# Kernel optimization log

Measured on AMD Instinct MI355X. Metric: run time of the kernel, lower is better.

## Reference

```python
import jax, jax.numpy as jnp
import numpy as np

LN_EPS = 1e-5
ATTN_THRESH = 0.0005


def _layernorm(x, g, b):
    mu = jnp.mean(x, axis=-1, keepdims=True)
    var = jnp.mean((x - mu) ** 2, axis=-1, keepdims=True)
    return (x - mu) / jnp.sqrt(var + LN_EPS) * g + b


def setup_inputs() -> dict:
    key = jax.random.key(0)
    ks = jax.random.split(key, 10)
    B, P, X, C = 4, 1024, 8192, 1024
    return {
        "feat": jax.random.normal(ks[0], (B, P, C), dtype=jnp.float32),
        "mem_k": jax.random.normal(ks[1], (B, X, C), dtype=jnp.float32),
        "mem_v": jax.random.normal(ks[2], (B, X, C), dtype=jnp.float32),
        "mem_c": jax.random.uniform(ks[3], (B, X, 1), dtype=jnp.float32),
        "mem_attn": jnp.zeros((B, X, 1), dtype=jnp.float32),
        "g_q": jax.random.uniform(ks[4], (C,), dtype=jnp.float32, minval=0.5, maxval=1.5),
        "b_q": jax.random.normal(ks[5], (C,), dtype=jnp.float32) * 0.02,
        "g_k": jax.random.uniform(ks[6], (C,), dtype=jnp.float32, minval=0.5, maxval=1.5),
        "b_k": jax.random.normal(ks[7], (C,), dtype=jnp.float32) * 0.02,
        "g_v": jax.random.uniform(ks[8], (C,), dtype=jnp.float32, minval=0.5, maxval=1.5),
        "b_v": jax.random.normal(ks[9], (C,), dtype=jnp.float32) * 0.02,
    }


def reference(feat, mem_k, mem_v, mem_c, mem_attn, g_q, b_q, g_k, b_k, g_v, b_v):
    # SpatialMemory.memory_read with res=True
    C = feat.shape[-1]
    q = _layernorm(feat, g_q, b_q)                      # [B,P,C]
    k = _layernorm(mem_k, g_k, b_k)                     # [B,X,C]
    affinity = jnp.einsum('bpc,bxc->bpx', q, k)
    affinity = affinity / jnp.sqrt(jnp.asarray(C, jnp.float32))
    # confidence scaling: mem_c viewed as [B,1,X]
    affinity = affinity * jnp.swapaxes(mem_c, 1, 2)
    attn = jax.nn.softmax(affinity, axis=-1)            # [B,P,X]
    # threshold sparsify + renormalize
    attn = jnp.where(attn < ATTN_THRESH, jnp.zeros((), attn.dtype), attn)
    attn = attn / jnp.sum(attn, axis=-1, keepdims=True)
    v = _layernorm(mem_v, g_v, b_v)                     # [B,X,C]
    out = jnp.einsum('bpx,bxc->bpc', attn, v) + feat    # residual
    return out
```

## Files before the change

kernel.cpp:

```cpp
#include <hip/hip_runtime.h>

typedef __attribute__((ext_vector_type(8))) _Float16 half8;
typedef __attribute__((ext_vector_type(4))) _Float16 half4v;
typedef __attribute__((ext_vector_type(4))) float f32x4;
typedef __attribute__((ext_vector_type(16))) float f32x16;

__device__ __forceinline__ void gll16(const void* g, void* l) {
  __builtin_amdgcn_global_load_lds(
      (const __attribute__((address_space(1))) unsigned int*)g,
      (__attribute__((address_space(3))) unsigned int*)l, 16, 0, 0);
}

__device__ __forceinline__ float h2f(unsigned short hb) {
  _Float16 h;
  __builtin_memcpy(&h, &hb, 2);
  return (float)h;
}

__global__ __launch_bounds__(256) void ln_cast_f16(
    const float* __restrict__ x, const float* __restrict__ g,
    const float* __restrict__ b, _Float16* __restrict__ y) {
  const int C = 1024;
  size_t row = blockIdx.x;
  int t = threadIdx.x;
  const float4* xr = (const float4*)(x + row * C);
  float4 v = xr[t];
  float s = v.x + v.y + v.z + v.w;
  float s2 = v.x * v.x + v.y * v.y + v.z * v.z + v.w * v.w;
#pragma unroll
  for (int off = 1; off < 64; off <<= 1) {
    s += __shfl_xor(s, off, 64);
    s2 += __shfl_xor(s2, off, 64);
  }
  __shared__ float ps[4], ps2[4];
  int wave = t >> 6, lane = t & 63;
  if (lane == 0) { ps[wave] = s; ps2[wave] = s2; }
  __syncthreads();
  s = ps[0] + ps[1] + ps[2] + ps[3];
  s2 = ps2[0] + ps2[1] + ps2[2] + ps2[3];
  float mu = s * (1.0f / C);
  float var = s2 * (1.0f / C) - mu * mu;
  float rstd = rsqrtf(var + 1e-5f);
  float4 gv = ((const float4*)g)[t];
  float4 bv = ((const float4*)b)[t];
  half4v o;
  o.x = (_Float16)((v.x - mu) * rstd * gv.x + bv.x);
  o.y = (_Float16)((v.y - mu) * rstd * gv.y + bv.y);
  o.z = (_Float16)((v.z - mu) * rstd * gv.z + bv.z);
  o.w = (_Float16)((v.w - mu) * rstd * gv.w + bv.w);
  ((half4v*)(y + row * C))[t] = o;
}

__global__ __launch_bounds__(256) void ln_cast_i8(
    const float* __restrict__ x, const float* __restrict__ g,
    const float* __restrict__ b, char* __restrict__ y,
    float* __restrict__ yscale) {
  const int C = 1024;
  size_t row = blockIdx.x;
  int t = threadIdx.x;
  const float4* xr = (const float4*)(x + row * C);
  float4 v = xr[t];
  float s = v.x + v.y + v.z + v.w;
  float s2 = v.x * v.x + v.y * v.y + v.z * v.z + v.w * v.w;
#pragma unroll
  for (int off = 1; off < 64; off <<= 1) {
    s += __shfl_xor(s, off, 64);
    s2 += __shfl_xor(s2, off, 64);
  }
  __shared__ float ps[4], ps2[4], pm[4];
  int wave = t >> 6, lane = t & 63;
  if (lane == 0) { ps[wave] = s; ps2[wave] = s2; }
  __syncthreads();
  s = ps[0] + ps[1] + ps[2] + ps[3];
  s2 = ps2[0] + ps2[1] + ps2[2] + ps2[3];
  float mu = s * (1.0f / C);
  float var = s2 * (1.0f / C) - mu * mu;
  float rstd = rsqrtf(var + 1e-5f);
  float4 gv = ((const float4*)g)[t];
  float4 bv = ((const float4*)b)[t];
  float o0 = (v.x - mu) * rstd * gv.x + bv.x;
  float o1 = (v.y - mu) * rstd * gv.y + bv.y;
  float o2 = (v.z - mu) * rstd * gv.z + bv.z;
  float o3 = (v.w - mu) * rstd * gv.w + bv.w;
  float mx = fmaxf(fmaxf(fabsf(o0), fabsf(o1)), fmaxf(fabsf(o2), fabsf(o3)));
#pragma unroll
  for (int off = 1; off < 64; off <<= 1) mx = fmaxf(mx, __shfl_xor(mx, off, 64));
  if (lane == 0) pm[wave] = mx;
  __syncthreads();
  mx = fmaxf(fmaxf(pm[0], pm[1]), fmaxf(pm[2], pm[3]));
  mx = fmaxf(mx, 1e-20f);
  float inv = 127.0f / mx;
  int q0 = (int)rintf(o0 * inv), q1 = (int)rintf(o1 * inv);
  int q2 = (int)rintf(o2 * inv), q3 = (int)rintf(o3 * inv);
  unsigned pk = ((unsigned)(q0 & 0xff)) | ((unsigned)(q1 & 0xff) << 8) |
                ((unsigned)(q2 & 0xff) << 16) | ((unsigned)(q3 & 0xff) << 24);
  ((unsigned*)(y + row * C))[t] = pk;
  if (t == 0) yscale[row] = mx * (1.0f / 127.0f);
}

__global__ __launch_bounds__(512, 2) void gemm_qk_256(
    const _Float16* __restrict__ A,
    const _Float16* __restrict__ Bm,
    _Float16* __restrict__ Sm,
    const float* __restrict__ conf)
{
  const int N = 8192, K = 1024;
  int bz = blockIdx.z;
  const _Float16* Ab = A + (size_t)bz * 1024 * K;
  const _Float16* Bb = Bm + (size_t)bz * (size_t)N * K;
  _Float16* Sb = Sm + (size_t)bz * 1024 * N;

  __shared__ _Float16 lA[4 * 8192];
  __shared__ _Float16 lB[4 * 8192];

  int tid = threadIdx.x;
  int wave = tid >> 6, lane = tid & 63;
  int wm = wave >> 2, wn = wave & 3;
  int lr = lane & 31, lk = lane >> 5;
  int m0 = blockIdx.y * 256, n0 = blockIdx.x * 256;

  f32x16 acc[4][2];
#pragma unroll
  for (int i = 0; i < 4; ++i)
#pragma unroll
    for (int j = 0; j < 2; ++j)
#pragma unroll
      for (int e = 0; e < 16; ++e) acc[i][j][e] = 0.f;

  int r = tid & 255, c0 = tid >> 8;
  const _Float16* gA = Ab + (size_t)(m0 + r) * K + c0 * 8;
  const _Float16* gB = Bb + (size_t)(n0 + r) * K + c0 * 8;
  int dA = c0 * 2048 + r * 8;

  auto stage = [&](int t) {
    int bo = (t & 3) * 8192;
    const _Float16* ga = gA + t * 32;
    const _Float16* gb = gB + t * 32;
    gll16(ga, &lA[bo + dA]);
    gll16(ga + 16, &lA[bo + dA + 4096]);
    gll16(gb, &lB[bo + dA]);
    gll16(gb + 16, &lB[bo + dA + 4096]);
  };

  auto compute = [&](int bo) {
#pragma unroll
    for (int ks = 0; ks < 2; ++ks) {
      const _Float16* la = &lA[bo + (ks * 2 + lk) * 2048 + (wm * 128 + lr) * 8];
      const _Float16* lb = &lB[bo + (ks * 2 + lk) * 2048 + (wn * 64 + lr) * 8];
      half8 a0 = *(const half8*)(la);
      half8 a1 = *(const half8*)(la + 256);
      half8 a2 = *(const half8*)(la + 512);
      half8 a3 = *(const half8*)(la + 768);
      half8 b0 = *(const half8*)(lb);
      half8 b1 = *(const half8*)(lb + 256);
      __builtin_amdgcn_s_setprio(1);
      acc[0][0] = __builtin_amdgcn_mfma_f32_32x32x16_f16(a0, b0, acc[0][0], 0, 0, 0);
      acc[1][0] = __builtin_amdgcn_mfma_f32_32x32x16_f16(a1, b0, acc[1][0], 0, 0, 0);
      acc[2][0] = __builtin_amdgcn_mfma_f32_32x32x16_f16(a2, b0, acc[2][0], 0, 0, 0);
      acc[3][0] = __builtin_amdgcn_mfma_f32_32x32x16_f16(a3, b0, acc[3][0], 0, 0, 0);
      acc[0][1] = __builtin_amdgcn_mfma_f32_32x32x16_f16(a0, b1, acc[0][1], 0, 0, 0);
      acc[1][1] = __builtin_amdgcn_mfma_f32_32x32x16_f16(a1, b1, acc[1][1], 0, 0, 0);
      acc[2][1] = __builtin_amdgcn_mfma_f32_32x32x16_f16(a2, b1, acc[2][1], 0, 0, 0);
      acc[3][1] = __builtin_amdgcn_mfma_f32_32x32x16_f16(a3, b1, acc[3][1], 0, 0, 0);
      __builtin_amdgcn_s_setprio(0);
    }
  };

  stage(0);
  stage(1);
  stage(2);

#pragma unroll 4
  for (int kt = 0; kt < 29; ++kt) {
    stage(kt + 3);
    __builtin_amdgcn_s_waitcnt(0xF7C);
    __builtin_amdgcn_s_barrier();
    __builtin_amdgcn_sched_barrier(0);
    compute((kt & 3) * 8192);
    __builtin_amdgcn_sched_barrier(0);
    __builtin_amdgcn_s_barrier();
  }
  __builtin_amdgcn_s_waitcnt(0xF78);
  __builtin_amdgcn_s_barrier();
  __builtin_amdgcn_sched_barrier(0);
  compute(1 * 8192);
  __builtin_amdgcn_sched_barrier(0);
  __builtin_amdgcn_s_barrier();
  __builtin_amdgcn_s_waitcnt(0xF74);
  __builtin_amdgcn_s_barrier();
  __builtin_amdgcn_sched_barrier(0);
  compute(2 * 8192);
  __builtin_amdgcn_sched_barrier(0);
  __builtin_amdgcn_s_barrier();
  __builtin_amdgcn_s_waitcnt(0xF70);
  __builtin_amdgcn_s_barrier();
  __builtin_amdgcn_sched_barrier(0);
  compute(3 * 8192);

  const float* cb = conf + (size_t)bz * N;
#pragma unroll
  for (int nf = 0; nf < 2; ++nf) {
    int gn = n0 + wn * 64 + nf * 32 + lr;
    float cs = 0.03125f * cb[gn];
#pragma unroll
    for (int mf = 0; mf < 4; ++mf) {
      int gmb = m0 + wm * 128 + mf * 32 + 4 * lk;
#pragma unroll
      for (int rr = 0; rr < 16; ++rr) {
        int gm = gmb + (rr & 3) + 8 * (rr >> 2);
        Sb[(size_t)gm * N + gn] = (_Float16)(acc[mf][nf][rr] * cs);
      }
    }
  }
}

__global__ __launch_bounds__(256) void softmax_compact(
    const _Float16* __restrict__ S, unsigned* __restrict__ entries,
    int* __restrict__ counts) {
  const int X = 8192;
  size_t row = blockIdx.x;
  const half8* sr = (const half8*)(S + row * X);
  int t = threadIdx.x;
  int wave = t >> 6, lane = t & 63;
  __shared__ float sh[4];
  __shared__ int scnt;

  float v[32];
#pragma unroll
  for (int j = 0; j < 4; ++j) {
    half8 h = sr[t + j * 256];
#pragma unroll
    for (int c = 0; c < 8; ++c) v[j * 8 + c] = (float)h[c];
  }

  float m = -1e30f;
#pragma unroll
  for (int i = 0; i < 32; ++i) m = fmaxf(m, v[i]);
#pragma unroll
  for (int off = 1; off < 64; off <<= 1) m = fmaxf(m, __shfl_xor(m, off, 64));
  if (lane == 0) sh[wave] = m;
  __syncthreads();
  m = fmaxf(fmaxf(sh[0], sh[1]), fmaxf(sh[2], sh[3]));
  __syncthreads();

  float l = 0.f;
#pragma unroll
  for (int i = 0; i < 32; ++i) {
    v[i] = __expf(v[i] - m);
    l += v[i];
  }
#pragma unroll
  for (int off = 1; off < 64; off <<= 1) l += __shfl_xor(l, off, 64);
  if (lane == 0) sh[wave] = l;
  __syncthreads();
  l = sh[0] + sh[1] + sh[2] + sh[3];
  __syncthreads();

  float thr = 0.0005f * l;
  float ks = 0.f;
#pragma unroll
  for (int i = 0; i < 32; ++i) {
    v[i] = (v[i] >= thr) ? v[i] : 0.f;
    ks += v[i];
  }
#pragma unroll
  for (int off = 1; off < 64; off <<= 1) ks += __shfl_xor(ks, off, 64);
  if (lane == 0) sh[wave] = ks;
  __syncthreads();
  if (t == 0) scnt = 0;
  __syncthreads();
  ks = sh[0] + sh[1] + sh[2] + sh[3];

  float inv = 1.0f / ks;
  unsigned* er = entries + row * 2048;
#pragma unroll
  for (int j = 0; j < 4; ++j) {
#pragma unroll
    for (int c = 0; c < 8; ++c) {
      float val = v[j * 8 + c];
      if (val > 0.f) {
        int pos = atomicAdd(&scnt, 1);
        _Float16 h = (_Float16)(val * inv);
        unsigned short hb;
        __builtin_memcpy(&hb, &h, 2);
        er[pos] = ((unsigned)((t + j * 256) * 8 + c) << 16) | hb;
      }
    }
  }
  __syncthreads();
  if (t == 0) counts[row] = scnt;
}

__device__ __forceinline__ void acc4(float* a, unsigned w, float wt) {
  a[0] += wt * (float)(signed char)(w & 0xff);
  a[1] += wt * (float)(signed char)((w >> 8) & 0xff);
  a[2] += wt * (float)(signed char)((w >> 16) & 0xff);
  a[3] += wt * (float)(signed char)(w >> 24);
}

__global__ __launch_bounds__(512) void gather_pv_i8(
    const unsigned* __restrict__ entries, const int* __restrict__ counts,
    const char* __restrict__ v8, const float* __restrict__ vscale,
    const float* __restrict__ feat, float* __restrict__ out) {
  const int X = 8192, C = 1024;
  int row = blockIdx.x;
  int b = row >> 10;
  int t = threadIdx.x;
  int s = t >> 6;
  int lane = t & 63;
  int c = lane * 16;

  __shared__ unsigned se[2048];
  __shared__ float red[8][1028];

  int cnt = counts[row];
  const unsigned* er = entries + (size_t)row * 2048;
  for (int i = t; i < cnt; i += 512) se[i] = er[i];
  __syncthreads();

  const char* vb = v8 + (size_t)b * X * C;
  const float* sb = vscale + (size_t)b * X;
  float a[16];
#pragma unroll
  for (int i = 0; i < 16; ++i) a[i] = 0.f;

#pragma unroll 2
  for (int j = s; j < cnt; j += 8) {
    unsigned e = se[j];
    int x = e >> 16;
    float w = h2f((unsigned short)(e & 0xffff)) * sb[x];
    uint4 pv = *(const uint4*)(vb + (size_t)x * C + c);
    acc4(a + 0, pv.x, w);
    acc4(a + 4, pv.y, w);
    acc4(a + 8, pv.z, w);
    acc4(a + 12, pv.w, w);
  }
  float* rp = &red[s][c];
#pragma unroll
  for (int i = 0; i < 16; ++i) rp[i] = a[i];
  __syncthreads();

  int p = t * 2;
  float2 f = *(const float2*)(feat + (size_t)row * C + p);
  float o0 = f.x, o1 = f.y;
#pragma unroll
  for (int ss = 0; ss < 8; ++ss) {
    o0 += red[ss][p];
    o1 += red[ss][p + 1];
  }
  float2 o = {o0, o1};
  *(float2*)(out + (size_t)row * C + p) = o;
}

extern "C" void kernel_launch(void* const* d_in, const int* in_sizes, int n_in,
                              void* d_out, int out_size, void* d_ws, size_t ws_size,
                              hipStream_t stream) {
  const int B = 4, P = 1024, X = 8192, C = 1024;
  const float* feat  = (const float*)d_in[0];
  const float* mem_k = (const float*)d_in[1];
  const float* mem_v = (const float*)d_in[2];
  const float* mem_c = (const float*)d_in[3];
  const float* g_q = (const float*)d_in[5];
  const float* b_q = (const float*)d_in[6];
  const float* g_k = (const float*)d_in[7];
  const float* b_k = (const float*)d_in[8];
  const float* g_v = (const float*)d_in[9];
  const float* b_v = (const float*)d_in[10];

  char* ws = (char*)d_ws;
  const size_t MB = 1024 * 1024;
  _Float16* q16 = (_Float16*)(ws + 0);
  _Float16* k16 = (_Float16*)(ws + 8 * MB);
  _Float16* S   = (_Float16*)(ws + 72 * MB);
  char*     v8  = (char*)(ws + 136 * MB);
  float* vscale = (float*)(ws + 168 * MB);
  unsigned* entries = (unsigned*)(ws + 169 * MB);
  int*      counts  = (int*)(ws + 201 * MB);

  ln_cast_f16<<<B * P, 256, 0, stream>>>(feat, g_q, b_q, q16);
  ln_cast_f16<<<B * X, 256, 0, stream>>>(mem_k, g_k, b_k, k16);
  ln_cast_i8<<<B * X, 256, 0, stream>>>(mem_v, g_v, b_v, v8, vscale);
  gemm_qk_256<<<dim3(X / 256, P / 256, B), 512, 0, stream>>>(q16, k16, S, mem_c);
  softmax_compact<<<B * P, 256, 0, stream>>>(S, entries, counts);
  gather_pv_i8<<<B * P, 512, 0, stream>>>(entries, counts, v8, vscale, feat,
                                          (float*)d_out);
}
```

Baseline: 504.1 us.

## Fuse layernorm kernels and merge softmax compaction into gather kernel

```diff
diff --git a/kernel.cpp b/kernel.cpp
--- a/kernel.cpp
+++ b/kernel.cpp
@@ -3,7 +3,6 @@
 typedef __attribute__((ext_vector_type(8))) _Float16 half8;
 typedef __attribute__((ext_vector_type(4))) _Float16 half4v;
 typedef __attribute__((ext_vector_type(4))) float f32x4;
-typedef __attribute__((ext_vector_type(16))) float f32x16;
 
 __device__ __forceinline__ void gll16(const void* g, void* l) {
   __builtin_amdgcn_global_load_lds(
@@ -11,91 +10,88 @@
       (__attribute__((address_space(3))) unsigned int*)l, 16, 0, 0);
 }
 
-__device__ __forceinline__ float h2f(unsigned short hb) {
-  _Float16 h;
-  __builtin_memcpy(&h, &hb, 2);
-  return (float)h;
-}
-
-__global__ __launch_bounds__(256) void ln_cast_f16(
-    const float* __restrict__ x, const float* __restrict__ g,
-    const float* __restrict__ b, _Float16* __restrict__ y) {
+__global__ __launch_bounds__(256) void ln_fused(
+    const float* __restrict__ feat, const float* __restrict__ mem_k,
+    const float* __restrict__ mem_v, const float* __restrict__ g_q,
+    const float* __restrict__ b_q, const float* __restrict__ g_k,
+    const float* __restrict__ b_k, const float* __restrict__ g_v,
+    const float* __restrict__ b_v, _Float16* __restrict__ q16,
+    _Float16* __restrict__ k16, char* __restrict__ v8,
+    float* __restrict__ vscale) {
   const int C = 1024;
-  size_t row = blockIdx.x;
-  int t = threadIdx.x;
+  int wave = threadIdx.x >> 6, lane = threadIdx.x & 63;
+  int task = blockIdx.x * 4 + wave;
+
+  const float *x, *g, *b;
+  int mode;
+  size_t row;
+  if (task < 4096) {
+    x = feat; g = g_q; b = b_q; mode = 0; row = task;
+  } else if (task < 36864) {
+    x = mem_k; g = g_k; b = b_k; mode = 1; row = task - 4096;
+  } else {
+    x = mem_v; g = g_v; b = b_v; mode = 2; row = task - 36864;
+  }
+
   const float4* xr = (const float4*)(x + row * C);
-  float4 v = xr[t];
-  float s = v.x + v.y + v.z + v.w;
-  float s2 = v.x * v.x + v.y * v.y + v.z * v.z + v.w * v.w;
+  float4 v[4];
+  float s = 0.f, s2 = 0.f;
+#pragma unroll
+  for (int j = 0; j < 4; ++j) {
+    v[j] = xr[lane + j * 64];
+    s += v[j].x + v[j].y + v[j].z + v[j].w;
+    s2 += v[j].x * v[j].x + v[j].y * v[j].y + v[j].z * v[j].z + v[j].w * v[j].w;
+  }
 #pragma unroll
   for (int off = 1; off < 64; off <<= 1) {
     s += __shfl_xor(s, off, 64);
     s2 += __shfl_xor(s2, off, 64);
   }
-  __shared__ float ps[4], ps2[4];
-  int wave = t >> 6, lane = t & 63;
-  if (lane == 0) { ps[wave] = s; ps2[wave] = s2; }
-  __syncthreads();
-  s = ps[0] + ps[1] + ps[2] + ps[3];
-  s2 = ps2[0] + ps2[1] + ps2[2] + ps2[3];
   float mu = s * (1.0f / C);
   float var = s2 * (1.0f / C) - mu * mu;
   float rstd = rsqrtf(var + 1e-5f);
-  float4 gv = ((const float4*)g)[t];
-  float4 bv = ((const float4*)b)[t];
-  half4v o;
-  o.x = (_Float16)((v.x - mu) * rstd * gv.x + bv.x);
-  o.y = (_Float16)((v.y - mu) * rstd * gv.y + bv.y);
-  o.z = (_Float16)((v.z - mu) * rstd * gv.z + bv.z);
-  o.w = (_Float16)((v.w - mu) * rstd * gv.w + bv.w);
-  ((half4v*)(y + row * C))[t] = o;
-}
-
-__global__ __launch_bounds__(256) void ln_cast_i8(
-    const float* __restrict__ x, const float* __restrict__ g,
-    const float* __restrict__ b, char* __restrict__ y,
-    float* __restrict__ yscale) {
-  const int C = 1024;
-  size_t row = blockIdx.x;
-  int t = threadIdx.x;
-  const float4* xr = (const float4*)(x + row * C);
-  float4 v = xr[t];
-  float s = v.x + v.y + v.z + v.w;
-  float s2 = v.x * v.x + v.y * v.y + v.z * v.z + v.w * v.w;
-#pragma unroll
-  for (int off = 1; off < 64; off <<= 1) {
-    s += __shfl_xor(s, off, 64);
-    s2 += __shfl_xor(s2, off, 64);
-  }
-  __shared__ float ps[4], ps2[4], pm[4];
-  int wave = t >> 6, lane = t & 63;
-  if (lane == 0) { ps[wave] = s; ps2[wave] = s2; }
-  __syncthreads();
-  s = ps[0] + ps[1] + ps[2] + ps[3];
-  s2 = ps2[0] + ps2[1] + ps2[2] + ps2[3];
-  float mu = s * (1.0f / C);
-  float var = s2 * (1.0f / C) - mu * mu;
-  float rstd = rsqrtf(var + 1e-5f);
-  float4 gv = ((const float4*)g)[t];
-  float4 bv = ((const float4*)b)[t];
-  float o0 = (v.x - mu) * rstd * gv.x + bv.x;
-  float o1 = (v.y - mu) * rstd * gv.y + bv.y;
-  float o2 = (v.z - mu) * rstd * gv.z + bv.z;
-  float o3 = (v.w - mu) * rstd * gv.w + bv.w;
-  float mx = fmaxf(fmaxf(fabsf(o0), fabsf(o1)), fmaxf(fabsf(o2), fabsf(o3)));
-#pragma unroll
-  for (int off = 1; off < 64; off <<= 1) mx = fmaxf(mx, __shfl_xor(mx, off, 64));
-  if (lane == 0) pm[wave] = mx;
-  __syncthreads();
-  mx = fmaxf(fmaxf(pm[0], pm[1]), fmaxf(pm[2], pm[3]));
-  mx = fmaxf(mx, 1e-20f);
-  float inv = 127.0f / mx;
-  int q0 = (int)rintf(o0 * inv), q1 = (int)rintf(o1 * inv);
-  int q2 = (int)rintf(o2 * inv), q3 = (int)rintf(o3 * inv);
-  unsigned pk = ((unsigned)(q0 & 0xff)) | ((unsigned)(q1 & 0xff) << 8) |
-                ((unsigned)(q2 & 0xff) << 16) | ((unsigned)(q3 & 0xff) << 24);
-  ((unsigned*)(y + row * C))[t] = pk;
-  if (t == 0) yscale[row] = mx * (1.0f / 127.0f);
+
+  float y[16];
+#pragma unroll
+  for (int j = 0; j < 4; ++j) {
+    float4 gv = ((const float4*)g)[lane + j * 64];
+    float4 bv = ((const float4*)b)[lane + j * 64];
+    y[4 * j + 0] = (v[j].x - mu) * rstd * gv.x + bv.x;
+    y[4 * j + 1] = (v[j].y - mu) * rstd * gv.y + bv.y;
+    y[4 * j + 2] = (v[j].z - mu) * rstd * gv.z + bv.z;
+    y[4 * j + 3] = (v[j].w - mu) * rstd * gv.w + bv.w;
+  }
+
+  if (mode < 2) {
+    _Float16* yo = (mode == 0 ? q16 : k16) + row * C;
+#pragma unroll
+    for (int j = 0; j < 4; ++j) {
+      half4v h;
+      h.x = (_Float16)y[4 * j + 0];
+      h.y = (_Float16)y[4 * j + 1];
+      h.z = (_Float16)y[4 * j + 2];
+      h.w = (_Float16)y[4 * j + 3];
+      ((half4v*)yo)[lane + j * 64] = h;
+    }
+  } else {
+    float mx = 0.f;
+#pragma unroll
+    for (int i = 0; i < 16; ++i) mx = fmaxf(mx, fabsf(y[i]));
+#pragma unroll
+    for (int off = 1; off < 64; off <<= 1) mx = fmaxf(mx, __shfl_xor(mx, off, 64));
+    mx = fmaxf(mx, 1e-20f);
+    float inv = 127.0f / mx;
+    unsigned* yo = (unsigned*)(v8 + row * C);
+#pragma unroll
+    for (int j = 0; j < 4; ++j) {
+      int q0 = (int)rintf(y[4 * j + 0] * inv), q1 = (int)rintf(y[4 * j + 1] * inv);
+      int q2 = (int)rintf(y[4 * j + 2] * inv), q3 = (int)rintf(y[4 * j + 3] * inv);
+      unsigned pk = ((unsigned)(q0 & 0xff)) | ((unsigned)(q1 & 0xff) << 8) |
+                    ((unsigned)(q2 & 0xff) << 16) | ((unsigned)(q3 & 0xff) << 24);
+      yo[lane + j * 64] = pk;
+    }
+    if (lane == 0) vscale[row] = mx * (1.0f / 127.0f);
+  }
 }
 
 __global__ __launch_bounds__(512, 2) void gemm_qk_256(
@@ -119,6 +115,7 @@
   int lr = lane & 31, lk = lane >> 5;
   int m0 = blockIdx.y * 256, n0 = blockIdx.x * 256;
 
+  typedef __attribute__((ext_vector_type(16))) float f32x16;
   f32x16 acc[4][2];
 #pragma unroll
   for (int i = 0; i < 4; ++i)
@@ -214,83 +211,6 @@
   }
 }
 
-__global__ __launch_bounds__(256) void softmax_compact(
-    const _Float16* __restrict__ S, unsigned* __restrict__ entries,
-    int* __restrict__ counts) {
-  const int X = 8192;
-  size_t row = blockIdx.x;
-  const half8* sr = (const half8*)(S + row * X);
-  int t = threadIdx.x;
-  int wave = t >> 6, lane = t & 63;
-  __shared__ float sh[4];
-  __shared__ int scnt;
-
-  float v[32];
-#pragma unroll
-  for (int j = 0; j < 4; ++j) {
-    half8 h = sr[t + j * 256];
-#pragma unroll
-    for (int c = 0; c < 8; ++c) v[j * 8 + c] = (float)h[c];
-  }
-
-  float m = -1e30f;
-#pragma unroll
-  for (int i = 0; i < 32; ++i) m = fmaxf(m, v[i]);
-#pragma unroll
-  for (int off = 1; off < 64; off <<= 1) m = fmaxf(m, __shfl_xor(m, off, 64));
-  if (lane == 0) sh[wave] = m;
-  __syncthreads();
-  m = fmaxf(fmaxf(sh[0], sh[1]), fmaxf(sh[2], sh[3]));
-  __syncthreads();
-
-  float l = 0.f;
-#pragma unroll
-  for (int i = 0; i < 32; ++i) {
-    v[i] = __expf(v[i] - m);
-    l += v[i];
-  }
-#pragma unroll
-  for (int off = 1; off < 64; off <<= 1) l += __shfl_xor(l, off, 64);
-  if (lane == 0) sh[wave] = l;
-  __syncthreads();
-  l = sh[0] + sh[1] + sh[2] + sh[3];
-  __syncthreads();
-
-  float thr = 0.0005f * l;
-  float ks = 0.f;
-#pragma unroll
-  for (int i = 0; i < 32; ++i) {
-    v[i] = (v[i] >= thr) ? v[i] : 0.f;
-    ks += v[i];
-  }
-#pragma unroll
-  for (int off = 1; off < 64; off <<= 1) ks += __shfl_xor(ks, off, 64);
-  if (lane == 0) sh[wave] = ks;
-  __syncthreads();
-  if (t == 0) scnt = 0;
-  __syncthreads();
-  ks = sh[0] + sh[1] + sh[2] + sh[3];
-
-  float inv = 1.0f / ks;
-  unsigned* er = entries + row * 2048;
-#pragma unroll
-  for (int j = 0; j < 4; ++j) {
-#pragma unroll
-    for (int c = 0; c < 8; ++c) {
-      float val = v[j * 8 + c];
-      if (val > 0.f) {
-        int pos = atomicAdd(&scnt, 1);
-        _Float16 h = (_Float16)(val * inv);
-        unsigned short hb;
-        __builtin_memcpy(&hb, &h, 2);
-        er[pos] = ((unsigned)((t + j * 256) * 8 + c) << 16) | hb;
-      }
-    }
-  }
-  __syncthreads();
-  if (t == 0) counts[row] = scnt;
-}
-
 __device__ __forceinline__ void acc4(float* a, unsigned w, float wt) {
   a[0] += wt * (float)(signed char)(w & 0xff);
   a[1] += wt * (float)(signed char)((w >> 8) & 0xff);
@@ -298,44 +218,104 @@
   a[3] += wt * (float)(signed char)(w >> 24);
 }
 
-__global__ __launch_bounds__(512) void gather_pv_i8(
-    const unsigned* __restrict__ entries, const int* __restrict__ counts,
-    const char* __restrict__ v8, const float* __restrict__ vscale,
-    const float* __restrict__ feat, float* __restrict__ out) {
+__global__ __launch_bounds__(512) void softmax_gather(
+    const _Float16* __restrict__ S, const char* __restrict__ v8,
+    const float* __restrict__ vscale, const float* __restrict__ feat,
+    float* __restrict__ out) {
   const int X = 8192, C = 1024;
   int row = blockIdx.x;
   int b = row >> 10;
   int t = threadIdx.x;
-  int s = t >> 6;
-  int lane = t & 63;
-  int c = lane * 16;
-
-  __shared__ unsigned se[2048];
+  int wave = t >> 6, lane = t & 63;
+
+  __shared__ float sh[8];
+  __shared__ int scnt;
+  __shared__ unsigned short sx[2048];
+  __shared__ float sw[2048];
   __shared__ float red[8][1028];
 
-  int cnt = counts[row];
-  const unsigned* er = entries + (size_t)row * 2048;
-  for (int i = t; i < cnt; i += 512) se[i] = er[i];
-  __syncthreads();
+  const half8* sr = (const half8*)(S + (size_t)row * X);
+  float v[16];
+#pragma unroll
+  for (int j = 0; j < 2; ++j) {
+    half8 h = sr[t + j * 512];
+#pragma unroll
+    for (int c = 0; c < 8; ++c) v[j * 8 + c] = (float)h[c];
+  }
+
+  float m = -1e30f;
+#pragma unroll
+  for (int i = 0; i < 16; ++i) m = fmaxf(m, v[i]);
+#pragma unroll
+  for (int off = 1; off < 64; off <<= 1) m = fmaxf(m, __shfl_xor(m, off, 64));
+  if (lane == 0) sh[wave] = m;
+  __syncthreads();
+  m = fmaxf(fmaxf(fmaxf(sh[0], sh[1]), fmaxf(sh[2], sh[3])),
+            fmaxf(fmaxf(sh[4], sh[5]), fmaxf(sh[6], sh[7])));
+  __syncthreads();
+
+  float l = 0.f;
+#pragma unroll
+  for (int i = 0; i < 16; ++i) {
+    v[i] = __expf(v[i] - m);
+    l += v[i];
+  }
+#pragma unroll
+  for (int off = 1; off < 64; off <<= 1) l += __shfl_xor(l, off, 64);
+  if (lane == 0) sh[wave] = l;
+  __syncthreads();
+  l = sh[0] + sh[1] + sh[2] + sh[3] + sh[4] + sh[5] + sh[6] + sh[7];
+  __syncthreads();
+
+  float thr = 0.0005f * l;
+  float ks = 0.f;
+#pragma unroll
+  for (int i = 0; i < 16; ++i) {
+    v[i] = (v[i] >= thr) ? v[i] : 0.f;
+    ks += v[i];
+  }
+#pragma unroll
+  for (int off = 1; off < 64; off <<= 1) ks += __shfl_xor(ks, off, 64);
+  if (lane == 0) sh[wave] = ks;
+  if (t == 0) scnt = 0;
+  __syncthreads();
+  ks = sh[0] + sh[1] + sh[2] + sh[3] + sh[4] + sh[5] + sh[6] + sh[7];
+
+  float inv = 1.0f / ks;
+  const float* sb = vscale + (size_t)b * X;
+#pragma unroll
+  for (int j = 0; j < 2; ++j) {
+#pragma unroll
+    for (int c = 0; c < 8; ++c) {
+      float val = v[j * 8 + c];
+      if (val > 0.f) {
+        int pos = atomicAdd(&scnt, 1);
+        int x = (t + j * 512) * 8 + c;
+        sx[pos] = (unsigned short)x;
+        sw[pos] = val * inv * sb[x];
+      }
+    }
+  }
+  __syncthreads();
+  int cnt = scnt;
 
   const char* vb = v8 + (size_t)b * X * C;
-  const float* sb = vscale + (size_t)b * X;
+  int cby = lane * 16;
   float a[16];
 #pragma unroll
   for (int i = 0; i < 16; ++i) a[i] = 0.f;
 
 #pragma unroll 2
-  for (int j = s; j < cnt; j += 8) {
-    unsigned e = se[j];
-    int x = e >> 16;
-    float w = h2f((unsigned short)(e & 0xffff)) * sb[x];
-    uint4 pv = *(const uint4*)(vb + (size_t)x * C + c);
+  for (int j = wave; j < cnt; j += 8) {
+    int x = sx[j];
+    float w = sw[j];
+    uint4 pv = *(const uint4*)(vb + (size_t)x * C + cby);
     acc4(a + 0, pv.x, w);
     acc4(a + 4, pv.y, w);
     acc4(a + 8, pv.z, w);
     acc4(a + 12, pv.w, w);
   }
-  float* rp = &red[s][c];
+  float* rp = &red[wave][cby];
 #pragma unroll
   for (int i = 0; i < 16; ++i) rp[i] = a[i];
   __syncthreads();
@@ -374,14 +354,9 @@
   _Float16* S   = (_Float16*)(ws + 72 * MB);
   char*     v8  = (char*)(ws + 136 * MB);
   float* vscale = (float*)(ws + 168 * MB);
-  unsigned* entries = (unsigned*)(ws + 169 * MB);
-  int*      counts  = (int*)(ws + 201 * MB);
-
-  ln_cast_f16<<<B * P, 256, 0, stream>>>(feat, g_q, b_q, q16);
-  ln_cast_f16<<<B * X, 256, 0, stream>>>(mem_k, g_k, b_k, k16);
-  ln_cast_i8<<<B * X, 256, 0, stream>>>(mem_v, g_v, b_v, v8, vscale);
+
+  ln_fused<<<(4096 + 32768 + 32768) / 4, 256, 0, stream>>>(
+      feat, mem_k, mem_v, g_q, b_q, g_k, b_k, g_v, b_v, q16, k16, v8, vscale);
   gemm_qk_256<<<dim3(X / 256, P / 256, B), 512, 0, stream>>>(q16, k16, S, mem_c);
-  softmax_compact<<<B * P, 256, 0, stream>>>(S, entries, counts);
-  gather_pv_i8<<<B * P, 512, 0, stream>>>(entries, counts, v8, vscale, feat,
-                                          (float*)d_out);
-}
+  softmax_gather<<<B * P, 512, 0, stream>>>(S, v8, vscale, feat, (float*)d_out);
+}
```

Result: no change. 501.1 us (-0.6%).
